# Performance work log

Measured on AMD Instinct MI355X. Metric: run time of the kernel, lower is better.

## Reference

```python
import jax, jax.numpy as jnp
import numpy as np

B, LC, LQ, D = 32, 2048, 256, 256


def setup_inputs() -> dict:
    key = jax.random.key(0)
    kc, kq, kcm, kqm, kw = jax.random.split(key, 5)
    context = jax.random.normal(kc, (B, LC, D), dtype=jnp.float32)
    query = jax.random.normal(kq, (B, LQ, D), dtype=jnp.float32)
    # True = masked (matches torch masked_fill semantics)
    context_mask = jax.random.randint(kcm, (B, LC), 0, 2).astype(bool)
    query_mask = jax.random.randint(kqm, (B, LQ), 0, 2).astype(bool)
    # nn.Linear(3*dim, 1, bias=False) weight, flattened to (3D,)
    w0 = jax.random.normal(kw, (3 * D,), dtype=jnp.float32) * (1.0 / np.sqrt(3 * D))
    return {"context": context, "query": query, "context_mask": context_mask,
            "query_mask": query_mask, "w0": w0}


def reference(context, query, context_mask, query_mask, w0):
    d = context.shape[-1]
    wc, wq, wm = w0[:d], w0[d:2 * d], w0[2 * d:]
    # trilinear sim: w0 . [c, q, c*q]  ==  c.wc + q.wq + (c*wm) q^T
    sc = context @ wc                                   # (B, Lc)
    sq = query @ wq                                     # (B, Lq)
    sim = sc[:, :, None] + sq[:, None, :] + jnp.einsum(
        'bcd,bqd->bcq', context * wm, query)            # (B, Lc, Lq)
    mask = context_mask[:, :, None] | query_mask[:, None, :]
    sim = jnp.where(mask, jnp.float32(-1e30), sim)
    S = jax.nn.softmax(sim, axis=-1)                    # row softmax over Lq
    SS = jax.nn.softmax(sim, axis=1)                    # col softmax over Lc
    S = jnp.nan_to_num(S)
    SS = jnp.nan_to_num(SS)
    A = jnp.einsum('bcq,bqd->bcd', S, query)            # (B, Lc, D)
    T = jnp.einsum('bkq,bkd->bqd', SS, context)         # SS^T @ context, (B, Lq, D)
    Bmat = jnp.einsum('bcq,bqd->bcd', S, T)             # (B, Lc, D)
    return (A, Bmat)
```

## Files before the change

### kernel.cpp

```cpp
#include <hip/hip_runtime.h>

#define B_  32
#define LC_ 2048
#define LQ_ 256
#define D_  256
#define NEGH (-30000.0f)

typedef _Float16 f16;
typedef _Float16 f16x4 __attribute__((ext_vector_type(4)));
typedef _Float16 f16x8 __attribute__((ext_vector_type(8)));
typedef float    f32x4 __attribute__((ext_vector_type(4)));

__global__ __launch_bounds__(256) void k_prep(
    const float* __restrict__ ctx, const float* __restrict__ qry,
    const float* __restrict__ w0, f16* __restrict__ ctx16,
    f16* __restrict__ qrywm16, float* __restrict__ sc, float* __restrict__ sq)
{
    const int lane = threadIdx.x & 63;
    const int wave = threadIdx.x >> 6;
    const int row  = blockIdx.x * 4 + wave;
    const int NC = B_ * LC_;
    if (row < NC) {
        float4 v = *(const float4*)(ctx + (long long)row * D_ + lane * 4);
        f16x4 h; h[0] = (f16)v.x; h[1] = (f16)v.y; h[2] = (f16)v.z; h[3] = (f16)v.w;
        *(f16x4*)(ctx16 + (long long)row * D_ + lane * 4) = h;
        float4 wc = *(const float4*)(w0 + lane * 4);
        float s = v.x*wc.x + v.y*wc.y + v.z*wc.z + v.w*wc.w;
        #pragma unroll
        for (int off = 32; off > 0; off >>= 1) s += __shfl_down(s, off, 64);
        if (lane == 0) sc[row] = s;
    } else {
        int r = row - NC;
        float4 v = *(const float4*)(qry + (long long)r * D_ + lane * 4);
        float4 wm = *(const float4*)(w0 + 2 * D_ + lane * 4);
        f16x4 h;
        h[0] = (f16)(v.x * wm.x); h[1] = (f16)(v.y * wm.y);
        h[2] = (f16)(v.z * wm.z); h[3] = (f16)(v.w * wm.w);
        *(f16x4*)(qrywm16 + (long long)r * D_ + lane * 4) = h;
        float4 wq = *(const float4*)(w0 + D_ + lane * 4);
        float s = v.x*wq.x + v.y*wq.y + v.z*wq.z + v.w*wq.w;
        #pragma unroll
        for (int off = 32; off > 0; off >>= 1) s += __shfl_down(s, off, 64);
        if (lane == 0) sq[r] = s;
    }
}

__global__ __launch_bounds__(256) void k_tq(
    const float* __restrict__ in, f16* __restrict__ out)
{
    __shared__ float tile[64 * 65];
    const int b = blockIdx.z;
    const int r0 = blockIdx.x * 64, c0 = blockIdx.y * 64;
    const int t = threadIdx.x;
    const float* ib = in + (long long)b * LQ_ * D_;
    #pragma unroll
    for (int p = 0; p < 4; ++p) {
        int r = (t >> 4) + p * 16;
        int cb = (t & 15) * 4;
        float4 v = *(const float4*)(ib + (long long)(r0 + r) * D_ + c0 + cb);
        tile[r * 65 + cb + 0] = v.x;
        tile[r * 65 + cb + 1] = v.y;
        tile[r * 65 + cb + 2] = v.z;
        tile[r * 65 + cb + 3] = v.w;
    }
    __syncthreads();
    f16* ob = out + (long long)b * 512 * LQ_;
    #pragma unroll
    for (int p = 0; p < 4; ++p) {
        int c = (t >> 4) + p * 16;
        int rb = (t & 15) * 4;
        f16x4 h;
        h[0] = (f16)tile[(rb + 0) * 65 + c];
        h[1] = (f16)tile[(rb + 1) * 65 + c];
        h[2] = (f16)tile[(rb + 2) * 65 + c];
        h[3] = (f16)tile[(rb + 3) * 65 + c];
        *(f16x4*)(ob + (long long)(c0 + c) * LQ_ + r0 + rb) = h;
    }
}

#define LDA1 40
__global__ __launch_bounds__(256) void k_g1(
    const f16* __restrict__ ctx16, const f16* __restrict__ qrywm16,
    const float* __restrict__ sc, const float* __restrict__ sq,
    const int* __restrict__ cmask, const int* __restrict__ qmask,
    f16* __restrict__ sim16)
{
    __shared__ f16 As[128 * LDA1];
    __shared__ f16 Bs[256 * LDA1];
    const int b = blockIdx.z;
    const int c0 = blockIdx.x * 128;
    const int t = threadIdx.x, lane = t & 63, wv = t >> 6;
    const int wm_off = (wv >> 1) * 64, wn_off = (wv & 1) * 128;
    const f16* Ab = ctx16 + ((long long)b * LC_ + c0) * D_;
    const f16* Bb = qrywm16 + (long long)b * LQ_ * D_;
    const int srow = t >> 2, scg = (t & 3) * 8;
    f32x4 acc[4][8] = {};
    for (int k0 = 0; k0 < D_; k0 += 32) {
        #pragma unroll
        for (int p = 0; p < 2; ++p) {
            int r = srow + p * 64;
            *(f16x8*)(As + r * LDA1 + scg) = *(const f16x8*)(Ab + (long long)r * D_ + k0 + scg);
        }
        #pragma unroll
        for (int p = 0; p < 4; ++p) {
            int r = srow + p * 64;
            *(f16x8*)(Bs + r * LDA1 + scg) = *(const f16x8*)(Bb + (long long)r * D_ + k0 + scg);
        }
        __syncthreads();
        f16x8 af[4], bf[8];
        #pragma unroll
        for (int i = 0; i < 4; ++i)
            af[i] = *(const f16x8*)(As + (wm_off + i * 16 + (lane & 15)) * LDA1 + (lane >> 4) * 8);
        #pragma unroll
        for (int j = 0; j < 8; ++j)
            bf[j] = *(const f16x8*)(Bs + (wn_off + j * 16 + (lane & 15)) * LDA1 + (lane >> 4) * 8);
        #pragma unroll
        for (int i = 0; i < 4; ++i)
            #pragma unroll
            for (int j = 0; j < 8; ++j)
                acc[i][j] = __builtin_amdgcn_mfma_f32_16x16x32_f16(af[i], bf[j], acc[i][j], 0, 0, 0);
        __syncthreads();
    }
    float sqv[8]; int qmv[8];
    #pragma unroll
    for (int j = 0; j < 8; ++j) {
        int q = wn_off + j * 16 + (lane & 15);
        sqv[j] = sq[b * LQ_ + q];
        qmv[j] = qmask[b * LQ_ + q];
    }
    #pragma unroll
    for (int i = 0; i < 4; ++i) {
        #pragma unroll
        for (int r = 0; r < 4; ++r) {
            int c = c0 + wm_off + i * 16 + (lane >> 4) * 4 + r;
            float scv = sc[b * LC_ + c];
            int cm = cmask[b * LC_ + c];
            f16* orow = sim16 + ((long long)b * LC_ + c) * LQ_ + wn_off + (lane & 15);
            #pragma unroll
            for (int j = 0; j < 8; ++j) {
                float val = (cm | qmv[j]) ? NEGH : (acc[i][j][r] + scv + sqv[j]);
                orow[j * 16] = (f16)val;
            }
        }
    }
}

__global__ __launch_bounds__(256) void k_s1(
    const f16* __restrict__ sim16, float* __restrict__ rowm, float* __restrict__ rowinvl,
    float* __restrict__ pm, float* __restrict__ pl)
{
    __shared__ float tile[32 * 260];
    const int ch = blockIdx.x;
    const int b  = blockIdx.y;
    const int t  = threadIdx.x;
    const int c0 = ch * 32;
    const f16* sb = sim16 + ((long long)b * LC_ + c0) * LQ_;
    #pragma unroll
    for (int p = 0; p < 8; ++p) {
        int r = p * 4 + (t >> 6);
        int cb = (t & 63) * 4;
        f16x4 v = *(const f16x4*)(sb + (long long)r * LQ_ + cb);
        tile[r * 260 + cb + 0] = (float)v[0];
        tile[r * 260 + cb + 1] = (float)v[1];
        tile[r * 260 + cb + 2] = (float)v[2];
        tile[r * 260 + cb + 3] = (float)v[3];
    }
    __syncthreads();
    {
        int r = t >> 3, s = t & 7;
        const float* rp = tile + r * 260;
        float m = -INFINITY;
        #pragma unroll
        for (int i = 0; i < 32; ++i) m = fmaxf(m, rp[(i << 3) + s]);
        m = fmaxf(m, __shfl_xor(m, 1, 64));
        m = fmaxf(m, __shfl_xor(m, 2, 64));
        m = fmaxf(m, __shfl_xor(m, 4, 64));
        float l = 0.f;
        #pragma unroll
        for (int i = 0; i < 32; ++i) l += __expf(rp[(i << 3) + s] - m);
        l += __shfl_xor(l, 1, 64);
        l += __shfl_xor(l, 2, 64);
        l += __shfl_xor(l, 4, 64);
        if (s == 0) {
            rowm[b * LC_ + c0 + r] = m;
            rowinvl[b * LC_ + c0 + r] = 1.0f / l;
        }
    }
    {
        float m = -INFINITY;
        #pragma unroll 8
        for (int r = 0; r < 32; ++r) m = fmaxf(m, tile[r * 260 + t]);
        float l = 0.f;
        #pragma unroll 8
        for (int r = 0; r < 32; ++r) l += __expf(tile[r * 260 + t] - m);
        int idx = (b * 64 + ch) * LQ_ + t;
        pm[idx] = m; pl[idx] = l;
    }
}

__global__ __launch_bounds__(256) void k_colreduce(
    const float* __restrict__ pm, const float* __restrict__ pl,
    float* __restrict__ colm, float* __restrict__ colinvl)
{
    const int col = blockIdx.x * 256 + threadIdx.x;
    const int b = col >> 8, q = col & 255;
    float M = -INFINITY, L = 0.f;
    for (int ch = 0; ch < 64; ++ch) {
        int idx = (b * 64 + ch) * LQ_ + q;
        float m = pm[idx], l = pl[idx];
        float nM = fmaxf(M, m);
        L = L * __expf(M - nM) + l * __expf(m - nM);
        M = nM;
    }
    colm[col] = M; colinvl[col] = 1.0f / L;
}

#define LDA3 66
__global__ __launch_bounds__(256) void k_g3(
    const f16* __restrict__ ctx16, const f16* __restrict__ sim16,
    const float* __restrict__ colm, const float* __restrict__ colinvl,
    f16* __restrict__ Bcat)
{
    __shared__ f16 As[128 * LDA3];
    __shared__ f16 Bs[64 * LDA3];
    __shared__ float colm_s[64], cil_s[64];
    const int b = blockIdx.x;
    const int combo = blockIdx.y;
    const int qt = combo & 3, dh = combo >> 2;
    const int q0 = qt * 64, d0 = dh * 128;
    const int t = threadIdx.x, lane = t & 63, wv = t >> 6;
    const int wm_off = (wv >> 1) * 64, wn_off = (wv & 1) * 32;
    if (t < 64) {
        colm_s[t] = colm[b * LQ_ + q0 + t];
        cil_s[t]  = colinvl[b * LQ_ + q0 + t];
    }
    __syncthreads();
    const f16* Ab = ctx16 + (long long)b * LC_ * D_;
    const f16* Sb = sim16 + (long long)b * LC_ * LQ_;
    f32x4 acc[4][2] = {};
    const int acc_ = t >> 4, ad8 = (t & 15) * 8;
    const int bcc = t >> 3, bq8 = (t & 7) * 8;
    for (int c0 = 0; c0 < LC_; c0 += 64) {
        #pragma unroll
        for (int p = 0; p < 4; ++p) {
            int cc = acc_ + p * 16;
            f16x8 h = *(const f16x8*)(Ab + (long long)(c0 + cc) * D_ + d0 + ad8);
            #pragma unroll
            for (int j = 0; j < 8; ++j)
                As[(ad8 + j) * LDA3 + cc] = h[j];
        }
        #pragma unroll
        for (int p = 0; p < 2; ++p) {
            int cc = bcc + p * 32;
            f16x8 h = *(const f16x8*)(Sb + (long long)(c0 + cc) * LQ_ + q0 + bq8);
            #pragma unroll
            for (int j = 0; j < 8; ++j)
                Bs[(bq8 + j) * LDA3 + cc] = (f16)__expf((float)h[j] - colm_s[bq8 + j]);
        }
        __syncthreads();
        #pragma unroll
        for (int kk = 0; kk < 64; kk += 32) {
            f16x8 af[4], bf[2];
            #pragma unroll
            for (int i = 0; i < 4; ++i)
                af[i] = *(const f16x8*)(As + (wm_off + i * 16 + (lane & 15)) * LDA3 + kk + (lane >> 4) * 8);
            #pragma unroll
            for (int j = 0; j < 2; ++j)
                bf[j] = *(const f16x8*)(Bs + (wn_off + j * 16 + (lane & 15)) * LDA3 + kk + (lane >> 4) * 8);
            #pragma unroll
            for (int i = 0; i < 4; ++i)
                #pragma unroll
                for (int j = 0; j < 2; ++j)
                    acc[i][j] = __builtin_amdgcn_mfma_f32_16x16x32_f16(af[i], bf[j], acc[i][j], 0, 0, 0);
        }
        __syncthreads();
    }
    #pragma unroll
    for (int i = 0; i < 4; ++i) {
        #pragma unroll
        for (int r = 0; r < 4; ++r) {
            int d = d0 + wm_off + i * 16 + (lane >> 4) * 4 + r;
            f16* orow = Bcat + (long long)b * 512 * LQ_ + (long long)(256 + d) * LQ_ + q0 + wn_off + (lane & 15);
            #pragma unroll
            for (int j = 0; j < 2; ++j)
                orow[j * 16] = (f16)(acc[i][j][r] * cil_s[wn_off + j * 16 + (lane & 15)]);
        }
    }
}

__global__ __launch_bounds__(256) void k_g23(
    const f16* __restrict__ sim16, const float* __restrict__ rowm,
    const float* __restrict__ rowinvl, const f16* __restrict__ Bcat,
    float* __restrict__ outA, float* __restrict__ outB)
{
    __shared__ f16 As[128 * LDA1];
    __shared__ f16 Bs[128 * LDA1];
    const int b = blockIdx.z;
    const int c0 = blockIdx.x * 128, n0 = blockIdx.y * 128;
    const int t = threadIdx.x, lane = t & 63, wv = t >> 6;
    const int wm_off = (wv >> 1) * 64, wn_off = (wv & 1) * 64;
    const f16* Ab = sim16 + ((long long)b * LC_ + c0) * LQ_;
    const f16* Bb = Bcat + ((long long)b * 512 + n0) * LQ_;
    const int srow = t >> 2, scg = (t & 3) * 8;
    float rm[2];
    #pragma unroll
    for (int p = 0; p < 2; ++p) rm[p] = rowm[b * LC_ + c0 + srow + p * 64];
    f32x4 acc[4][4] = {};
    for (int k0 = 0; k0 < LQ_; k0 += 32) {
        #pragma unroll
        for (int p = 0; p < 2; ++p) {
            int r = srow + p * 64;
            f16x8 h = *(const f16x8*)(Ab + (long long)r * LQ_ + k0 + scg);
            f16x8 e;
            #pragma unroll
            for (int j = 0; j < 8; ++j) e[j] = (f16)__expf((float)h[j] - rm[p]);
            *(f16x8*)(As + r * LDA1 + scg) = e;
            *(f16x8*)(Bs + r * LDA1 + scg) = *(const f16x8*)(Bb + (long long)r * LQ_ + k0 + scg);
        }
        __syncthreads();
        f16x8 af[4], bf[4];
        #pragma unroll
        for (int i = 0; i < 4; ++i)
            af[i] = *(const f16x8*)(As + (wm_off + i * 16 + (lane & 15)) * LDA1 + (lane >> 4) * 8);
        #pragma unroll
        for (int j = 0; j < 4; ++j)
            bf[j] = *(const f16x8*)(Bs + (wn_off + j * 16 + (lane & 15)) * LDA1 + (lane >> 4) * 8);
        #pragma unroll
        for (int i = 0; i < 4; ++i)
            #pragma unroll
            for (int j = 0; j < 4; ++j)
                acc[i][j] = __builtin_amdgcn_mfma_f32_16x16x32_f16(af[i], bf[j], acc[i][j], 0, 0, 0);
        __syncthreads();
    }
    float* outp = (n0 < 256) ? outA : outB;
    const int nbase = (n0 < 256) ? n0 : (n0 - 256);
    #pragma unroll
    for (int i = 0; i < 4; ++i) {
        #pragma unroll
        for (int r = 0; r < 4; ++r) {
            int c = c0 + wm_off + i * 16 + (lane >> 4) * 4 + r;
            float ri = rowinvl[b * LC_ + c];
            float* orow = outp + ((long long)b * LC_ + c) * D_ + nbase + wn_off + (lane & 15);
            #pragma unroll
            for (int j = 0; j < 4; ++j)
                orow[j * 16] = acc[i][j][r] * ri;
        }
    }
}

extern "C" void kernel_launch(void* const* d_in, const int* in_sizes, int n_in,
                              void* d_out, int out_size, void* d_ws, size_t ws_size,
                              hipStream_t stream) {
    const float* ctx   = (const float*)d_in[0];
    const float* qry   = (const float*)d_in[1];
    const int*   cmask = (const int*)d_in[2];
    const int*   qmask = (const int*)d_in[3];
    const float* w0    = (const float*)d_in[4];
    float* out = (float*)d_out;

    char* w = (char*)d_ws;
    float* sc      = (float*)w;  w += (long long)65536 * 4;
    float* sq      = (float*)w;  w += (long long)8192 * 4;
    float* rowm    = (float*)w;  w += (long long)65536 * 4;
    float* rowinvl = (float*)w;  w += (long long)65536 * 4;
    float* colm    = (float*)w;  w += (long long)8192 * 4;
    float* colinvl = (float*)w;  w += (long long)8192 * 4;
    float* pm      = (float*)w;  w += (long long)524288 * 4;
    float* pl      = (float*)w;  w += (long long)524288 * 4;
    f16*   sim16   = (f16*)w;    w += (long long)16777216 * 2;
    f16*   ctx16   = (f16*)w;    w += (long long)16777216 * 2;
    f16*   qrywm16 = (f16*)w;    w += (long long)2097152 * 2;
    f16*   Bcat    = (f16*)w;    w += (long long)4194304 * 2;

    k_prep<<<18432, 256, 0, stream>>>(ctx, qry, w0, ctx16, qrywm16, sc, sq);
    k_tq<<<dim3(4, 4, 32), 256, 0, stream>>>(qry, Bcat);
    k_g1<<<dim3(16, 1, 32), 256, 0, stream>>>(ctx16, qrywm16, sc, sq, cmask, qmask, sim16);
    k_s1<<<dim3(64, 32), 256, 0, stream>>>(sim16, rowm, rowinvl, pm, pl);
    k_colreduce<<<32, 256, 0, stream>>>(pm, pl, colm, colinvl);
    k_g3<<<dim3(32, 8), 256, 0, stream>>>(ctx16, sim16, colm, colinvl, Bcat);
    k_g23<<<dim3(16, 4, 32), 256, 0, stream>>>(sim16, rowm, rowinvl, Bcat,
        out, out + (long long)B_ * LC_ * D_);
}
```

Baseline: 327.6 us.

## Fuse softmax row/column statistics into sim GEMM epilogue and enlarge final GEMM tiles

```diff
diff --git a/kernel.cpp b/kernel.cpp
--- a/kernel.cpp
+++ b/kernel.cpp
@@ -83,10 +83,15 @@
     const f16* __restrict__ ctx16, const f16* __restrict__ qrywm16,
     const float* __restrict__ sc, const float* __restrict__ sq,
     const int* __restrict__ cmask, const int* __restrict__ qmask,
-    f16* __restrict__ sim16)
+    f16* __restrict__ sim16,
+    float* __restrict__ rowm, float* __restrict__ rowinvl,
+    float* __restrict__ pm, float* __restrict__ pl)
 {
     __shared__ f16 As[128 * LDA1];
     __shared__ f16 Bs[256 * LDA1];
+    __shared__ float rowpm[4][64], rowps[4][64];
+    __shared__ float colpm[4][128], colps[4][128];
+    __shared__ float rowmax_s[128], colmax_s[256];
     const int b = blockIdx.z;
     const int c0 = blockIdx.x * 128;
     const int t = threadIdx.x, lane = t & 63, wv = t >> 6;
@@ -128,73 +133,126 @@
         sqv[j] = sq[b * LQ_ + q];
         qmv[j] = qmask[b * LQ_ + q];
     }
+    float scv_[4][4]; int cmv_[4][4];
+    #pragma unroll
+    for (int i = 0; i < 4; ++i)
+        #pragma unroll
+        for (int r = 0; r < 4; ++r) {
+            int c = c0 + wm_off + i * 16 + (lane >> 4) * 4 + r;
+            scv_[i][r] = sc[b * LC_ + c];
+            cmv_[i][r] = cmask[b * LC_ + c];
+        }
+    float rmax[4][4], cmax[8];
+    #pragma unroll
+    for (int i = 0; i < 4; ++i)
+        #pragma unroll
+        for (int r = 0; r < 4; ++r) rmax[i][r] = -INFINITY;
+    #pragma unroll
+    for (int j = 0; j < 8; ++j) cmax[j] = -INFINITY;
     #pragma unroll
     for (int i = 0; i < 4; ++i) {
         #pragma unroll
         for (int r = 0; r < 4; ++r) {
             int c = c0 + wm_off + i * 16 + (lane >> 4) * 4 + r;
-            float scv = sc[b * LC_ + c];
-            int cm = cmask[b * LC_ + c];
             f16* orow = sim16 + ((long long)b * LC_ + c) * LQ_ + wn_off + (lane & 15);
             #pragma unroll
             for (int j = 0; j < 8; ++j) {
-                float val = (cm | qmv[j]) ? NEGH : (acc[i][j][r] + scv + sqv[j]);
-                orow[j * 16] = (f16)val;
+                float val = (cmv_[i][r] | qmv[j]) ? NEGH : (acc[i][j][r] + scv_[i][r] + sqv[j]);
+                f16 hh = (f16)val;
+                orow[j * 16] = hh;
+                float vr = (float)hh;
+                rmax[i][r] = fmaxf(rmax[i][r], vr);
+                cmax[j]    = fmaxf(cmax[j], vr);
             }
         }
     }
-}
-
-__global__ __launch_bounds__(256) void k_s1(
-    const f16* __restrict__ sim16, float* __restrict__ rowm, float* __restrict__ rowinvl,
-    float* __restrict__ pm, float* __restrict__ pl)
-{
-    __shared__ float tile[32 * 260];
-    const int ch = blockIdx.x;
-    const int b  = blockIdx.y;
-    const int t  = threadIdx.x;
-    const int c0 = ch * 32;
-    const f16* sb = sim16 + ((long long)b * LC_ + c0) * LQ_;
-    #pragma unroll
-    for (int p = 0; p < 8; ++p) {
-        int r = p * 4 + (t >> 6);
-        int cb = (t & 63) * 4;
-        f16x4 v = *(const f16x4*)(sb + (long long)r * LQ_ + cb);
-        tile[r * 260 + cb + 0] = (float)v[0];
-        tile[r * 260 + cb + 1] = (float)v[1];
-        tile[r * 260 + cb + 2] = (float)v[2];
-        tile[r * 260 + cb + 3] = (float)v[3];
+    #pragma unroll
+    for (int i = 0; i < 4; ++i)
+        #pragma unroll
+        for (int r = 0; r < 4; ++r) {
+            rmax[i][r] = fmaxf(rmax[i][r], __shfl_xor(rmax[i][r], 1, 64));
+            rmax[i][r] = fmaxf(rmax[i][r], __shfl_xor(rmax[i][r], 2, 64));
+            rmax[i][r] = fmaxf(rmax[i][r], __shfl_xor(rmax[i][r], 4, 64));
+            rmax[i][r] = fmaxf(rmax[i][r], __shfl_xor(rmax[i][r], 8, 64));
+        }
+    #pragma unroll
+    for (int j = 0; j < 8; ++j) {
+        cmax[j] = fmaxf(cmax[j], __shfl_xor(cmax[j], 16, 64));
+        cmax[j] = fmaxf(cmax[j], __shfl_xor(cmax[j], 32, 64));
+    }
+    if ((lane & 15) == 0) {
+        #pragma unroll
+        for (int i = 0; i < 4; ++i)
+            #pragma unroll
+            for (int r = 0; r < 4; ++r)
+                rowpm[wv][i * 16 + (lane >> 4) * 4 + r] = rmax[i][r];
+    }
+    if (lane < 16) {
+        #pragma unroll
+        for (int j = 0; j < 8; ++j) colpm[wv][j * 16 + lane] = cmax[j];
     }
     __syncthreads();
+    if (t < 128)
+        rowmax_s[t] = fmaxf(rowpm[2 * (t >> 6)][t & 63], rowpm[2 * (t >> 6) + 1][t & 63]);
+    colmax_s[t] = fmaxf(colpm[t >> 7][t & 127], colpm[(t >> 7) + 2][t & 127]);
+    __syncthreads();
+    float rmf[4][4], cmf[8];
+    #pragma unroll
+    for (int i = 0; i < 4; ++i)
+        #pragma unroll
+        for (int r = 0; r < 4; ++r)
+            rmf[i][r] = rowmax_s[wm_off + i * 16 + (lane >> 4) * 4 + r];
+    #pragma unroll
+    for (int j = 0; j < 8; ++j) cmf[j] = colmax_s[wn_off + j * 16 + (lane & 15)];
+    float rsum[4][4] = {}, csum[8] = {};
+    #pragma unroll
+    for (int i = 0; i < 4; ++i) {
+        #pragma unroll
+        for (int r = 0; r < 4; ++r) {
+            #pragma unroll
+            for (int j = 0; j < 8; ++j) {
+                float val = (cmv_[i][r] | qmv[j]) ? NEGH : (acc[i][j][r] + scv_[i][r] + sqv[j]);
+                float vr = (float)(f16)val;
+                rsum[i][r] += __expf(vr - rmf[i][r]);
+                csum[j]    += __expf(vr - cmf[j]);
+            }
+        }
+    }
+    #pragma unroll
+    for (int i = 0; i < 4; ++i)
+        #pragma unroll
+        for (int r = 0; r < 4; ++r) {
+            rsum[i][r] += __shfl_xor(rsum[i][r], 1, 64);
+            rsum[i][r] += __shfl_xor(rsum[i][r], 2, 64);
+            rsum[i][r] += __shfl_xor(rsum[i][r], 4, 64);
+            rsum[i][r] += __shfl_xor(rsum[i][r], 8, 64);
+        }
+    #pragma unroll
+    for (int j = 0; j < 8; ++j) {
+        csum[j] += __shfl_xor(csum[j], 16, 64);
+        csum[j] += __shfl_xor(csum[j], 32, 64);
+    }
+    if ((lane & 15) == 0) {
+        #pragma unroll
+        for (int i = 0; i < 4; ++i)
+            #pragma unroll
+            for (int r = 0; r < 4; ++r)
+                rowps[wv][i * 16 + (lane >> 4) * 4 + r] = rsum[i][r];
+    }
+    if (lane < 16) {
+        #pragma unroll
+        for (int j = 0; j < 8; ++j) colps[wv][j * 16 + lane] = csum[j];
+    }
+    __syncthreads();
+    if (t < 128) {
+        float l = rowps[2 * (t >> 6)][t & 63] + rowps[2 * (t >> 6) + 1][t & 63];
+        rowm[b * LC_ + c0 + t]    = rowmax_s[t];
+        rowinvl[b * LC_ + c0 + t] = 1.0f / l;
+    }
     {
-        int r = t >> 3, s = t & 7;
-        const float* rp = tile + r * 260;
-        float m = -INFINITY;
-        #pragma unroll
-        for (int i = 0; i < 32; ++i) m = fmaxf(m, rp[(i << 3) + s]);
-        m = fmaxf(m, __shfl_xor(m, 1, 64));
-        m = fmaxf(m, __shfl_xor(m, 2, 64));
-        m = fmaxf(m, __shfl_xor(m, 4, 64));
-        float l = 0.f;
-        #pragma unroll
-        for (int i = 0; i < 32; ++i) l += __expf(rp[(i << 3) + s] - m);
-        l += __shfl_xor(l, 1, 64);
-        l += __shfl_xor(l, 2, 64);
-        l += __shfl_xor(l, 4, 64);
-        if (s == 0) {
-            rowm[b * LC_ + c0 + r] = m;
-            rowinvl[b * LC_ + c0 + r] = 1.0f / l;
-        }
-    }
-    {
-        float m = -INFINITY;
-        #pragma unroll 8
-        for (int r = 0; r < 32; ++r) m = fmaxf(m, tile[r * 260 + t]);
-        float l = 0.f;
-        #pragma unroll 8
-        for (int r = 0; r < 32; ++r) l += __expf(tile[r * 260 + t] - m);
-        int idx = (b * 64 + ch) * LQ_ + t;
-        pm[idx] = m; pl[idx] = l;
+        int idx = (b * 16 + blockIdx.x) * LQ_ + t;
+        pm[idx] = colmax_s[t];
+        pl[idx] = colps[t >> 7][t & 127] + colps[(t >> 7) + 2][t & 127];
     }
 }
 
@@ -205,8 +263,8 @@
     const int col = blockIdx.x * 256 + threadIdx.x;
     const int b = col >> 8, q = col & 255;
     float M = -INFINITY, L = 0.f;
-    for (int ch = 0; ch < 64; ++ch) {
-        int idx = (b * 64 + ch) * LQ_ + q;
+    for (int ch = 0; ch < 16; ++ch) {
+        int idx = (b * 16 + ch) * LQ_ + q;
         float m = pm[idx], l = pl[idx];
         float nM = fmaxf(M, m);
         L = L * __expf(M - nM) + l * __expf(m - nM);
@@ -288,28 +346,29 @@
     }
 }
 
-__global__ __launch_bounds__(256) void k_g23(
+__global__ __launch_bounds__(512) void k_g23(
     const f16* __restrict__ sim16, const float* __restrict__ rowm,
     const float* __restrict__ rowinvl, const f16* __restrict__ Bcat,
     float* __restrict__ outA, float* __restrict__ outB)
 {
-    __shared__ f16 As[128 * LDA1];
-    __shared__ f16 Bs[128 * LDA1];
+    __shared__ f16 As[256 * LDA1];
+    __shared__ f16 Bs[256 * LDA1];
     const int b = blockIdx.z;
-    const int c0 = blockIdx.x * 128, n0 = blockIdx.y * 128;
+    const int c0 = blockIdx.x * 256, n0 = blockIdx.y * 256;
     const int t = threadIdx.x, lane = t & 63, wv = t >> 6;
-    const int wm_off = (wv >> 1) * 64, wn_off = (wv & 1) * 64;
+    const int wm_off = (wv >> 2) * 128;
+    const int wn_off = (wv & 3) * 64;
     const f16* Ab = sim16 + ((long long)b * LC_ + c0) * LQ_;
     const f16* Bb = Bcat + ((long long)b * 512 + n0) * LQ_;
     const int srow = t >> 2, scg = (t & 3) * 8;
     float rm[2];
     #pragma unroll
-    for (int p = 0; p < 2; ++p) rm[p] = rowm[b * LC_ + c0 + srow + p * 64];
-    f32x4 acc[4][4] = {};
+    for (int p = 0; p < 2; ++p) rm[p] = rowm[b * LC_ + c0 + srow + p * 128];
+    f32x4 acc[8][4] = {};
     for (int k0 = 0; k0 < LQ_; k0 += 32) {
         #pragma unroll
         for (int p = 0; p < 2; ++p) {
-            int r = srow + p * 64;
+            int r = srow + p * 128;
             f16x8 h = *(const f16x8*)(Ab + (long long)r * LQ_ + k0 + scg);
             f16x8 e;
             #pragma unroll
@@ -318,29 +377,27 @@
             *(f16x8*)(Bs + r * LDA1 + scg) = *(const f16x8*)(Bb + (long long)r * LQ_ + k0 + scg);
         }
         __syncthreads();
-        f16x8 af[4], bf[4];
-        #pragma unroll
-        for (int i = 0; i < 4; ++i)
-            af[i] = *(const f16x8*)(As + (wm_off + i * 16 + (lane & 15)) * LDA1 + (lane >> 4) * 8);
+        f16x8 bf[4];
         #pragma unroll
         for (int j = 0; j < 4; ++j)
             bf[j] = *(const f16x8*)(Bs + (wn_off + j * 16 + (lane & 15)) * LDA1 + (lane >> 4) * 8);
         #pragma unroll
-        for (int i = 0; i < 4; ++i)
+        for (int i = 0; i < 8; ++i) {
+            f16x8 af = *(const f16x8*)(As + (wm_off + i * 16 + (lane & 15)) * LDA1 + (lane >> 4) * 8);
             #pragma unroll
             for (int j = 0; j < 4; ++j)
-                acc[i][j] = __builtin_amdgcn_mfma_f32_16x16x32_f16(af[i], bf[j], acc[i][j], 0, 0, 0);
-        __syncthreads();
-    }
-    float* outp = (n0 < 256) ? outA : outB;
-    const int nbase = (n0 < 256) ? n0 : (n0 - 256);
-    #pragma unroll
-    for (int i = 0; i < 4; ++i) {
+                acc[i][j] = __builtin_amdgcn_mfma_f32_16x16x32_f16(af, bf[j], acc[i][j], 0, 0, 0);
+        }
+        __syncthreads();
+    }
+    float* outp = (n0 == 0) ? outA : outB;
+    #pragma unroll
+    for (int i = 0; i < 8; ++i) {
         #pragma unroll
         for (int r = 0; r < 4; ++r) {
             int c = c0 + wm_off + i * 16 + (lane >> 4) * 4 + r;
             float ri = rowinvl[b * LC_ + c];
-            float* orow = outp + ((long long)b * LC_ + c) * D_ + nbase + wn_off + (lane & 15);
+            float* orow = outp + ((long long)b * LC_ + c) * D_ + wn_off + (lane & 15);
             #pragma unroll
             for (int j = 0; j < 4; ++j)
                 orow[j * 16] = acc[i][j][r] * ri;
@@ -374,10 +431,10 @@
 
     k_prep<<<18432, 256, 0, stream>>>(ctx, qry, w0, ctx16, qrywm16, sc, sq);
     k_tq<<<dim3(4, 4, 32), 256, 0, stream>>>(qry, Bcat);
-    k_g1<<<dim3(16, 1, 32), 256, 0, stream>>>(ctx16, qrywm16, sc, sq, cmask, qmask, sim16);
-    k_s1<<<dim3(64, 32), 256, 0, stream>>>(sim16, rowm, rowinvl, pm, pl);
+    k_g1<<<dim3(16, 1, 32), 256, 0, stream>>>(ctx16, qrywm16, sc, sq, cmask, qmask,
+        sim16, rowm, rowinvl, pm, pl);
     k_colreduce<<<32, 256, 0, stream>>>(pm, pl, colm, colinvl);
     k_g3<<<dim3(32, 8), 256, 0, stream>>>(ctx16, sim16, colm, colinvl, Bcat);
-    k_g23<<<dim3(16, 4, 32), 256, 0, stream>>>(sim16, rowm, rowinvl, Bcat,
+    k_g23<<<dim3(8, 2, 32), 512, 0, stream>>>(sim16, rowm, rowinvl, Bcat,
         out, out + (long long)B_ * LC_ * D_);
 }
```

After: 320.9 us. -2.1%, faster.
